# Kernel tuning notes

Measured on AMD Instinct MI355X. Metric: run time of the kernel, lower is better.

The kernel has to match this reference:

```python
import jax, jax.numpy as jnp
import numpy as np

L, D, N = 2048, 1024, 16

def _inverse_softplus(x):
    return x + jnp.log(-jnp.expm1(-x))

def setup_inputs() -> dict:
    key = jax.random.key(0)
    ks = jax.random.split(key, 8)
    xs = jax.random.normal(ks[0], (L, D), dtype=jnp.float32)
    # Dense(N) applied to xs[..., None]: kernel [1, N]
    WB = jax.random.normal(ks[1], (1, N), dtype=jnp.float32)
    bB = jnp.zeros((N,), dtype=jnp.float32)
    WC = jax.random.normal(ks[2], (1, N), dtype=jnp.float32)
    bC = jnp.zeros((N,), dtype=jnp.float32)
    # Dense(1) over channel dim: kernel [D, 1]; small scale keeps softplus(Delta) sane
    WD = 0.01 * jax.random.normal(ks[3], (D, 1), dtype=jnp.float32)
    bD = jnp.zeros((1,), dtype=jnp.float32)
    # s4d_real_initializer: log(arange(N)+1) tiled over D
    log_neg_Adiag = jnp.tile(jnp.log(jnp.arange(N, dtype=jnp.float32) + 1.0), (D, 1))
    # delta initializer: inverse_softplus of log-uniform dt in [1e-3, 1]
    dt_min, dt_max = 0.001, 1.0
    u = jax.random.uniform(ks[4], (D,), dtype=jnp.float32)
    dt = jnp.exp(u * (jnp.log(dt_max) - jnp.log(dt_min)) + jnp.log(dt_min))
    delta_param = _inverse_softplus(dt)
    return {"xs": xs, "WB": WB, "bB": bB, "WC": WC, "bC": bC,
            "WD": WD, "bD": bD, "log_neg_Adiag": log_neg_Adiag,
            "delta_param": delta_param}

def _scan_op(a, b):
    Ai, Bxi = a
    Aj, Bxj = b
    return (Aj * Ai, Aj * Bxi + Bxj)

def reference(xs, WB, bB, WC, bC, WD, bD, log_neg_Adiag, delta_param):
    # selective params: Bs, Cs [L, D, N]; Delta [L, D]
    Bs = xs[..., None] * WB[0] + bB
    Cs = xs[..., None] * WC[0] + bC
    Delta = jax.nn.softplus(delta_param + (xs @ WD + bD))  # [L,1] broadcasts over [D]
    # discretize
    Adiag = -jnp.exp(log_neg_Adiag)                 # [D, N]
    log_Abar = Delta[..., None] * Adiag             # [L, D, N]
    Abar = jnp.exp(log_Abar)
    Bbar = (Abar - 1.0) / log_Abar * Delta[..., None] * Bs
    Bxs = Bbar * xs[..., None]
    # associative scan over positions (axis 0)
    _, hs = jax.lax.associative_scan(_scan_op, (Abar, Bxs))
    ys = jnp.sum(hs * Cs, axis=-1)                  # [L, D]
    return ys, hs
```

## Files before the change

### kernel.cpp

```cpp
#include <hip/hip_runtime.h>

#define Lr 2048
#define Dr 1024
#define Nr 16
#define Gc 32
#define LC (Lr/Gc)
#define DN (Dr*Nr)
#define GDN (Gc*DN)

#define LOG2E 1.442695041f
#define LN2   0.69314718056f

typedef float f32x4 __attribute__((ext_vector_type(4)));

__device__ __forceinline__ float exp2_hw(float x){ return __builtin_amdgcn_exp2f(x); }
__device__ __forceinline__ float log2_hw(float x){ return __builtin_amdgcn_logf(x); }
__device__ __forceinline__ float exp_hw(float x) { return exp2_hw(x*LOG2E); }
__device__ __forceinline__ float softplus_fast(float x){
  float t = exp2_hw(-LOG2E*fabsf(x));
  return fmaxf(x, 0.f) + LN2*log2_hw(1.f + t);
}

__global__ void k_rowdot(const float* __restrict__ xs, const float* __restrict__ WD,
                         const float* __restrict__ bD, float* __restrict__ z){
  int l = blockIdx.x;
  const float4* row = (const float4*)(xs + (size_t)l*Dr);
  const float4* w4  = (const float4*)WD;
  int i = threadIdx.x;
  float4 a = row[i], b = w4[i];
  float s = fmaf(a.x,b.x, fmaf(a.y,b.y, fmaf(a.z,b.z, a.w*b.w)));
  #pragma unroll
  for (int off = 32; off > 0; off >>= 1) s += __shfl_down(s, off, 64);
  __shared__ float red[4];
  int wid = threadIdx.x >> 6, lane = threadIdx.x & 63;
  if (lane == 0) red[wid] = s;
  __syncthreads();
  if (threadIdx.x == 0) z[l] = red[0] + red[1] + red[2] + red[3] + bD[0];
}

__global__ __launch_bounds__(256) void k_phase1(
    const float* __restrict__ xs, const float* __restrict__ WB,
    const float* __restrict__ bB,
    const float* __restrict__ lnA, const float* __restrict__ dparam,
    const float* __restrict__ z,
    float* __restrict__ aggA, float* __restrict__ aggB){
  int t  = blockIdx.x*256 + threadIdx.x;
  int g  = t >> 12;
  int r  = t & 4095;
  int d  = r >> 2;
  int n4 = r & 3;
  float4 la = *(const float4*)(lnA + d*Nr + n4*4);
  float4 wb = *(const float4*)(WB  + n4*4);
  float4 bb = *(const float4*)(bB  + n4*4);
  float lav[4] = {la.x,la.y,la.z,la.w};
  float wbv[4] = {wb.x,wb.y,wb.z,wb.w};
  float bbv[4] = {bb.x,bb.y,bb.z,bb.w};
  float ad2[4], p[4], q[4], Ap[4], Bc[4];
  #pragma unroll
  for (int j=0;j<4;j++){
    float a = -exp_hw(lav[j]);
    ad2[j] = a*LOG2E;
    float ia = 1.f/a;
    p[j]=wbv[j]*ia; q[j]=bbv[j]*ia; Ap[j]=1.f; Bc[j]=0.f;
  }
  float dp = dparam[d];
  int l0 = g*LC;
  #pragma unroll 2
  for (int i=0;i<LC;i++){
    int l = l0+i;
    float x  = xs[(size_t)l*Dr + d];
    float dl = softplus_fast(dp + z[l]);
    float x2 = x*x;
    #pragma unroll
    for (int j=0;j<4;j++){
      float Ab = exp2_hw(dl*ad2[j]);
      float Bx = (Ab-1.f)*fmaf(x2, p[j], x*q[j]);
      Ap[j] *= Ab;
      Bc[j] = fmaf(Ab, Bc[j], Bx);
    }
  }
  *(float4*)(aggA + (size_t)g*DN + d*Nr + n4*4) = make_float4(Ap[0],Ap[1],Ap[2],Ap[3]);
  *(float4*)(aggB + (size_t)g*DN + d*Nr + n4*4) = make_float4(Bc[0],Bc[1],Bc[2],Bc[3]);
}

__global__ __launch_bounds__(64) void k_carry(
    const float* __restrict__ aggA, const float* __restrict__ aggB,
    float* __restrict__ carry){
  const int t = blockIdx.x*64 + threadIdx.x;
  float h = 0.f;
  for (int g0 = 0; g0 < Gc; g0 += 16){
    float A_[16], B_[16];
    #pragma unroll
    for (int k=0;k<16;k++){
      A_[k] = aggA[(size_t)(g0+k)*DN + t];
      B_[k] = aggB[(size_t)(g0+k)*DN + t];
    }
    #pragma unroll
    for (int k=0;k<16;k++){
      carry[(size_t)(g0+k)*DN + t] = h;
      h = fmaf(A_[k], h, B_[k]);
    }
  }
}

__global__ __launch_bounds__(256) void k_phase3(
    const float* __restrict__ xs, const float* __restrict__ WB,
    const float* __restrict__ bB, const float* __restrict__ WC,
    const float* __restrict__ bC,
    const float* __restrict__ lnA, const float* __restrict__ dparam,
    const float* __restrict__ z, const float* __restrict__ carry,
    float* __restrict__ ys, float* __restrict__ hs){
  int t  = blockIdx.x*256 + threadIdx.x;
  int g  = t >> 12;
  int r  = t & 4095;
  int d  = r >> 2;
  int n4 = r & 3;
  float4 la = *(const float4*)(lnA + d*Nr + n4*4);
  float4 wb = *(const float4*)(WB  + n4*4);
  float4 bb = *(const float4*)(bB  + n4*4);
  float4 wcv= *(const float4*)(WC  + n4*4);
  float4 bcv= *(const float4*)(bC  + n4*4);
  float4 h0 = *(const float4*)(carry + (size_t)g*DN + d*Nr + n4*4);
  float lav[4] = {la.x,la.y,la.z,la.w};
  float wbv[4] = {wb.x,wb.y,wb.z,wb.w};
  float bbv[4] = {bb.x,bb.y,bb.z,bb.w};
  float wc[4]  = {wcv.x,wcv.y,wcv.z,wcv.w};
  float bc[4]  = {bcv.x,bcv.y,bcv.z,bcv.w};
  float h[4]   = {h0.x,h0.y,h0.z,h0.w};
  float ad2[4], p[4], q[4];
  #pragma unroll
  for (int j=0;j<4;j++){
    float a = -exp_hw(lav[j]);
    ad2[j] = a*LOG2E;
    float ia = 1.f/a;
    p[j]=wbv[j]*ia; q[j]=bbv[j]*ia;
  }
  float dp = dparam[d];
  int l0 = g*LC;
  #pragma unroll 2
  for (int i=0;i<LC;i++){
    int l = l0+i;
    float x  = xs[(size_t)l*Dr + d];
    float dl = softplus_fast(dp + z[l]);
    float x2 = x*x;
    float y = 0.f;
    #pragma unroll
    for (int j=0;j<4;j++){
      float Ab = exp2_hw(dl*ad2[j]);
      float Bx = (Ab-1.f)*fmaf(x2, p[j], x*q[j]);
      h[j] = fmaf(Ab, h[j], Bx);
      y = fmaf(h[j], fmaf(x, wc[j], bc[j]), y);
    }
    f32x4 hv = {h[0],h[1],h[2],h[3]};
    __builtin_nontemporal_store(hv, (f32x4*)(hs + (size_t)l*DN + d*Nr + n4*4));
    y += __shfl_xor(y, 1, 64);
    y += __shfl_xor(y, 2, 64);
    if (n4 == 0) __builtin_nontemporal_store(y, &ys[(size_t)l*Dr + d]);
  }
}

extern "C" void kernel_launch(void* const* d_in, const int* in_sizes, int n_in,
                              void* d_out, int out_size, void* d_ws, size_t ws_size,
                              hipStream_t stream) {
  const float* xs     = (const float*)d_in[0];
  const float* WB     = (const float*)d_in[1];
  const float* bB     = (const float*)d_in[2];
  const float* WC     = (const float*)d_in[3];
  const float* bC     = (const float*)d_in[4];
  const float* WD     = (const float*)d_in[5];
  const float* bD     = (const float*)d_in[6];
  const float* lnA    = (const float*)d_in[7];
  const float* dparam = (const float*)d_in[8];

  float* ys = (float*)d_out;
  float* hs = ys + (size_t)Lr*Dr;

  float* z     = (float*)d_ws;
  float* aggA  = z + Lr;
  float* aggB  = aggA + GDN;
  float* carry = aggB + GDN;

  k_rowdot<<<Lr, 256, 0, stream>>>(xs, WD, bD, z);
  k_phase1<<<(Gc*Dr*4)/256, 256, 0, stream>>>(xs, WB, bB, lnA, dparam, z, aggA, aggB);
  k_carry<<<DN/64, 64, 0, stream>>>(aggA, aggB, carry);
  k_phase3<<<(Gc*Dr*4)/256, 256, 0, stream>>>(xs, WB, bB, WC, bC, lnA, dparam, z, carry, ys, hs);
}
```

Baseline: 66.68 us.

## Give each phase-3 thread all 16 states of one channel and double chunk count

Phase 3 now assigns one thread per (chunk, channel) holding all 16 state elements, instead of four threads each holding four. This removes the cross-lane shuffle reduction for ys and the redundant per-position xs and softplus work across the four lanes. The chunk count doubles to restore parallelism, which also doubles the phase-1 aggregate traffic and the sequential carry length. Each thread now issues four strided 16-byte hs stores per position. The stores are no longer contiguous across lanes, so write coalescing may suffer, and register pressure rises.

```diff
diff --git a/kernel.cpp b/kernel.cpp
--- a/kernel.cpp
+++ b/kernel.cpp
@@ -3,7 +3,7 @@
 #define Lr 2048
 #define Dr 1024
 #define Nr 16
-#define Gc 32
+#define Gc 64
 #define LC (Lr/Gc)
 #define DN (Dr*Nr)
 #define GDN (Gc*DN)
@@ -110,34 +110,35 @@
     const float* __restrict__ lnA, const float* __restrict__ dparam,
     const float* __restrict__ z, const float* __restrict__ carry,
     float* __restrict__ ys, float* __restrict__ hs){
-  int t  = blockIdx.x*256 + threadIdx.x;
-  int g  = t >> 12;
-  int r  = t & 4095;
-  int d  = r >> 2;
-  int n4 = r & 3;
-  float4 la = *(const float4*)(lnA + d*Nr + n4*4);
-  float4 wb = *(const float4*)(WB  + n4*4);
-  float4 bb = *(const float4*)(bB  + n4*4);
-  float4 wcv= *(const float4*)(WC  + n4*4);
-  float4 bcv= *(const float4*)(bC  + n4*4);
-  float4 h0 = *(const float4*)(carry + (size_t)g*DN + d*Nr + n4*4);
-  float lav[4] = {la.x,la.y,la.z,la.w};
-  float wbv[4] = {wb.x,wb.y,wb.z,wb.w};
-  float bbv[4] = {bb.x,bb.y,bb.z,bb.w};
-  float wc[4]  = {wcv.x,wcv.y,wcv.z,wcv.w};
-  float bc[4]  = {bcv.x,bcv.y,bcv.z,bcv.w};
-  float h[4]   = {h0.x,h0.y,h0.z,h0.w};
-  float ad2[4], p[4], q[4];
-  #pragma unroll
-  for (int j=0;j<4;j++){
-    float a = -exp_hw(lav[j]);
-    ad2[j] = a*LOG2E;
-    float ia = 1.f/a;
-    p[j]=wbv[j]*ia; q[j]=bbv[j]*ia;
+  int tid = blockIdx.x*256 + threadIdx.x;
+  int d   = tid & (Dr-1);
+  int g   = tid >> 10;
+  float ad2[16], p[16], q[16], wc[16], bc[16], h[16];
+  {
+    const f32x4* lap = (const f32x4*)(lnA + d*Nr);
+    const f32x4* cp  = (const f32x4*)(carry + (size_t)g*DN + d*Nr);
+    const f32x4* wbp = (const f32x4*)WB;
+    const f32x4* bbp = (const f32x4*)bB;
+    const f32x4* wcp = (const f32x4*)WC;
+    const f32x4* bcp = (const f32x4*)bC;
+    #pragma unroll
+    for (int v=0; v<4; v++){
+      f32x4 lav = lap[v], hv = cp[v], wbv = wbp[v], bbv = bbp[v];
+      f32x4 wcv = wcp[v], bcv = bcp[v];
+      #pragma unroll
+      for (int e=0; e<4; e++){
+        int j = v*4+e;
+        float a = -exp_hw(lav[e]);
+        ad2[j] = a*LOG2E;
+        float ia = 1.f/a;
+        p[j] = wbv[e]*ia; q[j] = bbv[e]*ia;
+        wc[j] = wcv[e]; bc[j] = bcv[e];
+        h[j] = hv[e];
+      }
+    }
   }
-  float dp = dparam[d];
-  int l0 = g*LC;
-  #pragma unroll 2
+  const float dp = dparam[d];
+  const int l0 = g*LC;
   for (int i=0;i<LC;i++){
     int l = l0+i;
     float x  = xs[(size_t)l*Dr + d];
@@ -145,17 +146,19 @@
     float x2 = x*x;
     float y = 0.f;
     #pragma unroll
-    for (int j=0;j<4;j++){
+    for (int j=0;j<16;j++){
       float Ab = exp2_hw(dl*ad2[j]);
       float Bx = (Ab-1.f)*fmaf(x2, p[j], x*q[j]);
       h[j] = fmaf(Ab, h[j], Bx);
       y = fmaf(h[j], fmaf(x, wc[j], bc[j]), y);
     }
-    f32x4 hv = {h[0],h[1],h[2],h[3]};
-    __builtin_nontemporal_store(hv, (f32x4*)(hs + (size_t)l*DN + d*Nr + n4*4));
-    y += __shfl_xor(y, 1, 64);
-    y += __shfl_xor(y, 2, 64);
-    if (n4 == 0) __builtin_nontemporal_store(y, &ys[(size_t)l*Dr + d]);
+    float* hp = hs + (size_t)l*DN + d*Nr;
+    #pragma unroll
+    for (int v=0; v<4; v++){
+      f32x4 hv = {h[v*4+0],h[v*4+1],h[v*4+2],h[v*4+3]};
+      __builtin_nontemporal_store(hv, (f32x4*)(hp + v*4));
+    }
+    __builtin_nontemporal_store(y, ys + (size_t)l*Dr + d);
   }
 }
 
@@ -183,5 +186,5 @@
   k_rowdot<<<Lr, 256, 0, stream>>>(xs, WD, bD, z);
   k_phase1<<<(Gc*Dr*4)/256, 256, 0, stream>>>(xs, WB, bB, lnA, dparam, z, aggA, aggB);
   k_carry<<<DN/64, 64, 0, stream>>>(aggA, aggB, carry);
-  k_phase3<<<(Gc*Dr*4)/256, 256, 0, stream>>>(xs, WB, bB, WC, bC, lnA, dparam, z, carry, ys, hs);
+  k_phase3<<<(Gc*Dr)/256, 256, 0, stream>>>(xs, WB, bB, WC, bC, lnA, dparam, z, carry, ys, hs);
 }
```

Result: slower. 156.4 us (+134.5%).
